# Optimization experiments

Hardware: AMD Instinct MI355X
Metric: run time of the kernel (lower is better)

The kernel has to match this reference:

```python
import jax, jax.numpy as jnp
import numpy as np

N, C, H, W = 8, 32, 48, 48
S, K, OC = 2, 3, 32  # scale_int, kernel_size, out_channels
HID = 256
FEAT = C * K * K  # 288


def setup_inputs() -> dict:
    key = jax.random.key(0)
    ks = jax.random.split(key, 5)
    F_LR = jax.random.normal(ks[0], (N, C, H, W), dtype=jnp.float32)
    v = jax.random.normal(ks[1], (H * S * W * S, 3), dtype=jnp.float32)
    w1 = jax.random.normal(ks[2], (3, HID), dtype=jnp.float32) * 0.2
    b1 = jnp.zeros((HID,), dtype=jnp.float32)
    w2 = jax.random.normal(ks[3], (HID, FEAT * OC), dtype=jnp.float32) * 0.02
    b2 = jnp.zeros((FEAT * OC,), dtype=jnp.float32)
    return {"F_LR": F_LR, "v": v, "w1": w1, "b1": b1, "w2": w2, "b2": b2}


def _unfold(x, k):
    # torch F.unfold(x, k, padding=1): (N, C*k*k, H*W), channel-major then (ki,kj)
    n, c, h, w = x.shape
    xp = jnp.pad(x, ((0, 0), (0, 0), (1, 1), (1, 1)))
    cols = [xp[:, :, i:i + h, j:j + w] for i in range(k) for j in range(k)]
    p = jnp.stack(cols, axis=2)  # (N, C, k*k, H, W)
    return p.reshape(n, c * k * k, h * w)


def reference(F_LR, v, w1, b1, w2, b2):
    n = F_LR.shape[0]
    # weight prediction MLP
    hmid = jax.nn.relu(v @ w1 + b1)
    W_pred = hmid @ w2 + b2  # (H*S*W*S, C*K*K*OC)
    # reshape like torch: view(H,S,W,S,FEAT,OC).permute(1,3,0,2,4,5) -> (S*S, H*W, FEAT, OC)
    Wt = (W_pred.reshape(H, S, W, S, FEAT, OC)
          .transpose(1, 3, 0, 2, 4, 5)
          .reshape(S * S, H * W, FEAT, OC))
    # add_dimensions replicates F_LR S*S times, so patches are shared across p
    pat = _unfold(F_LR, K)  # (N, FEAT, H*W)
    # per-pixel tiny matmul: out[n,p,l,o] = sum_f pat[n,f,l] * Wt[p,l,f,o]
    out = jnp.einsum('nfl,plfo->nplo', pat, Wt)  # (N, S*S, H*W, OC)
    # assemble upsampled image: p=(sh,sw), pixel (h*S+sh, w*S+sw)
    out = (out.reshape(n, S, S, H, W, OC)
           .transpose(0, 5, 3, 1, 4, 2)
           .reshape(n, OC, S * H, S * W))
    # integer scale => create_mask is all-True, masked_select is identity
    return out
```

## Files before the change

kernel.cpp:

```cpp
#include <hip/hip_runtime.h>
#include <hip/hip_bf16.h>

#define NN    8
#define CC    32
#define HH    48
#define WW    48
#define OCC   32
#define HID   256
#define FEAT  288
#define RTOT  9216
#define COLS  9216
#define XUP   96
#define YUP   96
#define OUTSZ (NN*OCC*XUP*YUP)

using bf16x8 = __attribute__((ext_vector_type(8))) __bf16;
using bf16x4 = __attribute__((ext_vector_type(4))) __bf16;
using f32x4  = __attribute__((ext_vector_type(4))) float;

#define GLOAD_LDS16(gp, lp)                                                        \
  __builtin_amdgcn_global_load_lds((const __attribute__((address_space(1))) void*)(gp), \
                                   (__attribute__((address_space(3))) void*)(lp), 16, 0, 0)

__global__ void prep_hmid(const float* __restrict__ v, const float* __restrict__ w1,
                          const float* __restrict__ b1, __hip_bfloat16* __restrict__ hmidp) {
  int r = blockIdx.x;
  int t = threadIdx.x;
  float v0 = v[r*3+0], v1 = v[r*3+1], v2 = v[r*3+2];
  float val = v0*w1[t] + v1*w1[HID+t] + v2*w1[2*HID+t] + b1[t];
  val = fmaxf(val, 0.0f);
  int dst = ((r>>4)*8 + (t>>5))*512 + ((t>>3)&3)*128 + (r&15)*8 + (t&7);
  hmidp[dst] = __float2bfloat16(val);
}

__global__ void prep_w2(const float* __restrict__ w2, __hip_bfloat16* __restrict__ w2p) {
  int idx = blockIdx.x*256 + threadIdx.x;
  int k   = idx / COLS;
  int col = idx % COLS;
  float val = w2[idx];
  int colchunk = col >> 7;
  int cg   = (col >> 4) & 7;
  int lane = (((k>>3)&3)<<4) | (col & 15);
  int kb   = k >> 5;
  int i    = k & 7;
  int dst  = (((colchunk*8 + kb)*8 + cg)*64 + lane)*8 + i;
  w2p[dst] = __float2bfloat16(val);
}

__launch_bounds__(256, 2)
__global__ void fused_main(const float* __restrict__ F_LR,
                           const __hip_bfloat16* __restrict__ hmidp,
                           const __hip_bfloat16* __restrict__ w2p,
                           const float* __restrict__ b2,
                           float* __restrict__ outp,
                           int G, int nch) {
  __shared__ __align__(16) __bf16 pat[CC][3][18][NN];
  __shared__ __align__(16) float  wc[4*OCC*32];
  __shared__ __align__(16) __bf16 Bring[4*4096];
  __shared__ __align__(16) float  biasb[256];
  __shared__ __align__(16) char   dummy[2048];

  const int tid  = threadIdx.x;
  const int lane = tid & 63;
  const int wv   = tid >> 6;
  const int blk  = blockIdx.x;
  const int rowtile = blk / G;
  const int g       = blk - rowtile*G;
  const int X  = rowtile / 3;
  const int Yh = rowtile - X*3;
  const int h  = X >> 1;
  const int w0 = Yh * 16;
  const int l15 = lane & 15;
  const int qt  = lane >> 4;
  const int oc  = lane & 31;
  const int nh  = lane >> 5;
  const int colchunk0 = g*nch;
  const int NT = nch*8;

  const char* w2base = (const char*)w2p + (size_t)colchunk0*65536;
  char* BringB = (char*)Bring;
  auto stage_any = [&](int t) {
    if (t < NT) {
      const char* src = w2base + (size_t)t*8192 + wv*2048 + lane*16;
      char* dst = BringB + (t&3)*8192 + wv*2048;
      GLOAD_LDS16(src, dst);
      GLOAD_LDS16(src + 1024, dst + 1024);
    } else {
      const char* src = w2base + wv*2048 + lane*16;
      GLOAD_LDS16(src, (char*)dummy);
      GLOAD_LDS16(src + 1024, (char*)dummy + 1024);
    }
  };
  stage_any(0); stage_any(1); stage_any(2);
  asm volatile("" ::: "memory");

  bf16x8 a[2][8];
  {
    const bf16x8* ap = reinterpret_cast<const bf16x8*>(hmidp) + (size_t)rowtile*1024 + lane;
    #pragma unroll
    for (int mg = 0; mg < 2; ++mg)
      #pragma unroll
      for (int kb = 0; kb < 8; ++kb) a[mg][kb] = ap[(mg*8 + kb)*64];
  }

  {
    const int n = tid >> 5, c = tid & 31;
    const float* fsrc = F_LR + ((size_t)(n*CC + c)*HH)*WW;
    #pragma unroll
    for (int ki = 0; ki < 3; ++ki) {
      int hh = h - 1 + ki;
      bool hok = (unsigned)hh < (unsigned)HH;
      #pragma unroll
      for (int wi = 0; wi < 18; ++wi) {
        int ww = w0 - 1 + wi;
        float val = (hok && (unsigned)ww < (unsigned)WW) ? fsrc[hh*WW + ww] : 0.f;
        pat[c][ki][wi][n] = (__bf16)val;
      }
    }
  }
  asm volatile("s_waitcnt lgkmcnt(0)" ::: "memory");
  __builtin_amdgcn_sched_barrier(0);
  __builtin_amdgcn_s_barrier();

  float oacc[8][4];
  #pragma unroll
  for (int i = 0; i < 8; ++i)
    { oacc[i][0]=0.f; oacc[i][1]=0.f; oacc[i][2]=0.f; oacc[i][3]=0.f; }

  for (int ch = 0; ch < nch; ++ch) {
    if ((ch & 1) == 0) {
      const char* bsrc = (const char*)(b2 + (size_t)(colchunk0 + ch)*128) + lane*16;
      GLOAD_LDS16(bsrc, (char*)biasb);
    }

    f32x4 acc00 = {0,0,0,0}, acc01 = {0,0,0,0}, acc10 = {0,0,0,0}, acc11 = {0,0,0,0};

    #pragma unroll
    for (int s = 0; s < 8; ++s) {
      const int t = ch*8 + s;
      asm volatile("s_waitcnt vmcnt(4)" ::: "memory");
      const char* bufp = BringB + (size_t)(t&3)*8192 + wv*2048;
      bf16x8 b0 = *(const bf16x8*)(bufp + lane*16);
      bf16x8 b1 = *(const bf16x8*)(bufp + 1024 + lane*16);
      stage_any(t + 3);
      acc00 = __builtin_amdgcn_mfma_f32_16x16x32_bf16(a[0][s], b0, acc00, 0,0,0);
      acc01 = __builtin_amdgcn_mfma_f32_16x16x32_bf16(a[0][s], b1, acc01, 0,0,0);
      acc10 = __builtin_amdgcn_mfma_f32_16x16x32_bf16(a[1][s], b0, acc10, 0,0,0);
      acc11 = __builtin_amdgcn_mfma_f32_16x16x32_bf16(a[1][s], b1, acc11, 0,0,0);
    }

    asm volatile("s_waitcnt vmcnt(6)" ::: "memory");
    {
      float bias0 = biasb[(ch&1)*128 + wv*32 + l15];
      float bias1 = biasb[(ch&1)*128 + wv*32 + 16 + l15];
      #pragma unroll
      for (int mg = 0; mg < 2; ++mg) {
        #pragma unroll
        for (int ng = 0; ng < 2; ++ng) {
          f32x4 A = (mg==0) ? (ng==0?acc00:acc01) : (ng==0?acc10:acc11);
          float bb = ng ? bias1 : bias0;
          A[0]+=bb; A[1]+=bb; A[2]+=bb; A[3]+=bb;
          int ocx  = ng*16 + l15;
          int ridx = (mg*16 + qt*4) ^ ((ocx&7)<<2);
          *(f32x4*)&wc[wv*1024 + ocx*32 + ridx] = A;
        }
      }
    }
    asm volatile("s_waitcnt lgkmcnt(0)" ::: "memory");
    __builtin_amdgcn_sched_barrier(0);
    __builtin_amdgcn_s_barrier();

    const int swz = (oc & 7) << 2;
    #pragma unroll
    for (int fl = 0; fl < 4; ++fl) {
      const int f   = (colchunk0 + ch)*4 + fl;
      const int c   = f / 9;
      const int rem = f - c*9;
      const int ki  = rem / 3;
      const int kj  = rem - ki*3;
      const f32x4 wlo = *(const f32x4*)&wc[fl*1024 + oc*32 + ((wv*8    ) ^ swz)];
      const f32x4 whi = *(const f32x4*)&wc[fl*1024 + oc*32 + ((wv*8 + 4) ^ swz)];
      const __bf16* pbase = &pat[c][ki][0][0] + nh*4;
      #pragma unroll
      for (int rrh = 0; rrh < 4; ++rrh) {
        bf16x4 pq = *(const bf16x4*)(pbase + (wv*4 + rrh + kj)*8);
        float w0v = (rrh < 2) ? ((rrh == 0) ? wlo[0] : wlo[2]) : ((rrh == 2) ? whi[0] : whi[2]);
        float w1v = (rrh < 2) ? ((rrh == 0) ? wlo[1] : wlo[3]) : ((rrh == 2) ? whi[1] : whi[3]);
        #pragma unroll
        for (int q = 0; q < 4; ++q) {
          float pv = (float)pq[q];
          oacc[rrh*2][q]   += w0v * pv;
          oacc[rrh*2+1][q] += w1v * pv;
        }
      }
    }
    asm volatile("s_waitcnt lgkmcnt(0)" ::: "memory");
    __builtin_amdgcn_sched_barrier(0);
    __builtin_amdgcn_s_barrier();
  }

  float* OP = outp + (size_t)g*OUTSZ;
  #pragma unroll
  for (int q = 0; q < 4; ++q) {
    int n = nh*4 + q;
    f32x4 v0, v1;
    v0[0]=oacc[0][q]; v0[1]=oacc[1][q]; v0[2]=oacc[2][q]; v0[3]=oacc[3][q];
    v1[0]=oacc[4][q]; v1[1]=oacc[5][q]; v1[2]=oacc[6][q]; v1[3]=oacc[7][q];
    float* dst = OP + (((size_t)(n*OCC + oc)*XUP + X)*YUP + Yh*32 + wv*8);
    *(f32x4*)dst     = v0;
    *(f32x4*)(dst+4) = v1;
  }
}

__global__ void reduce2(const float* __restrict__ P, float* __restrict__ out) {
  int i = blockIdx.x*256 + threadIdx.x;
  if (i < OUTSZ/4) {
    f32x4 a = ((const f32x4*)P)[i];
    f32x4 b = ((const f32x4*)(P + OUTSZ))[i];
    ((f32x4*)out)[i] = a + b;
  }
}

extern "C" void kernel_launch(void* const* d_in, const int* in_sizes, int n_in,
                              void* d_out, int out_size, void* d_ws, size_t ws_size,
                              hipStream_t stream) {
  const float* F_LR = (const float*)d_in[0];
  const float* v    = (const float*)d_in[1];
  const float* w1   = (const float*)d_in[2];
  const float* b1   = (const float*)d_in[3];
  const float* w2   = (const float*)d_in[4];
  const float* b2   = (const float*)d_in[5];
  float* out = (float*)d_out;

  const size_t prepBytes = (size_t)RTOT*HID*2;
  const size_t need2 = 2*prepBytes + 2ull*OUTSZ*4;
  const int G   = (ws_size >= need2) ? 2 : 1;
  const int nch = 72 / G;

  __hip_bfloat16* hmidp = (__hip_bfloat16*)d_ws;
  __hip_bfloat16* w2p   = (__hip_bfloat16*)((char*)d_ws + prepBytes);
  float* P = (float*)((char*)d_ws + 2*prepBytes);
  float* target = (G == 2) ? P : out;

  hipLaunchKernelGGL(prep_hmid, dim3(RTOT), dim3(HID), 0, stream, v, w1, b1, hmidp);
  hipLaunchKernelGGL(prep_w2,   dim3((HID*COLS)/256), dim3(256), 0, stream, w2, w2p);
  hipLaunchKernelGGL(fused_main, dim3(288*G), dim3(256), 0, stream,
                     F_LR, hmidp, w2p, b2, target, G, nch);
  if (G == 2)
    hipLaunchKernelGGL(reduce2, dim3(OUTSZ/4/256), dim3(256), 0, stream, P, out);
}
```

Before: 199.9 us.

## Software-pipeline LDS B loads, raise MFMA priority, pack FMAs, coalesce patch staging

Restructures the MFMA inner loop so each step's B fragments are read from LDS one step ahead into double-buffered registers. The next global-to-LDS stage is issued after the MFMAs, and the MFMA group runs under raised wave priority. The per-pixel FMA accumulation uses 2-wide float vectors so the compiler can emit packed FMA, and patch loading becomes a flat strided loop for more coalesced global reads. The aim is to hide LDS latency behind MFMA work and cut ALU instruction count. In exchange it uses more registers and relies on delicate waitcnt counts, which could be off and cause stalls or races.

```diff
diff --git a/kernel.cpp b/kernel.cpp
--- a/kernel.cpp
+++ b/kernel.cpp
@@ -17,6 +17,7 @@
 using bf16x8 = __attribute__((ext_vector_type(8))) __bf16;
 using bf16x4 = __attribute__((ext_vector_type(4))) __bf16;
 using f32x4  = __attribute__((ext_vector_type(4))) float;
+using f32x2  = __attribute__((ext_vector_type(2))) float;
 
 #define GLOAD_LDS16(gp, lp)                                                        \
   __builtin_amdgcn_global_load_lds((const __attribute__((address_space(1))) void*)(gp), \
@@ -103,31 +104,34 @@
       for (int kb = 0; kb < 8; ++kb) a[mg][kb] = ap[(mg*8 + kb)*64];
   }
 
-  {
-    const int n = tid >> 5, c = tid & 31;
-    const float* fsrc = F_LR + ((size_t)(n*CC + c)*HH)*WW;
-    #pragma unroll
-    for (int ki = 0; ki < 3; ++ki) {
-      int hh = h - 1 + ki;
-      bool hok = (unsigned)hh < (unsigned)HH;
-      #pragma unroll
-      for (int wi = 0; wi < 18; ++wi) {
-        int ww = w0 - 1 + wi;
-        float val = (hok && (unsigned)ww < (unsigned)WW) ? fsrc[hh*WW + ww] : 0.f;
-        pat[c][ki][wi][n] = (__bf16)val;
-      }
-    }
+  for (int idx = tid; idx < NN*CC*3*18; idx += 256) {
+    int wi = idx % 18;
+    int t2 = idx / 18;
+    int ki = t2 % 3;
+    int t3 = t2 / 3;
+    int c  = t3 & 31;
+    int n  = t3 >> 5;
+    int hh = h - 1 + ki;
+    int ww = w0 - 1 + wi;
+    float val = 0.f;
+    if ((unsigned)hh < (unsigned)HH && (unsigned)ww < (unsigned)WW)
+      val = F_LR[((n*CC + c)*HH + hh)*WW + ww];
+    pat[c][ki][wi][n] = (__bf16)val;
   }
   asm volatile("s_waitcnt lgkmcnt(0)" ::: "memory");
   __builtin_amdgcn_sched_barrier(0);
   __builtin_amdgcn_s_barrier();
 
-  float oacc[8][4];
+  f32x2 oacc2[8][2];
   #pragma unroll
-  for (int i = 0; i < 8; ++i)
-    { oacc[i][0]=0.f; oacc[i][1]=0.f; oacc[i][2]=0.f; oacc[i][3]=0.f; }
+  for (int i = 0; i < 8; ++i) { oacc2[i][0] = 0.f; oacc2[i][1] = 0.f; }
+
+  auto ldb = [&](int u, int off) -> bf16x8 {
+    return *(const bf16x8*)(BringB + (size_t)(u&3)*8192 + wv*2048 + off + lane*16);
+  };
 
   for (int ch = 0; ch < nch; ++ch) {
+    const int t0 = ch*8;
     if ((ch & 1) == 0) {
       const char* bsrc = (const char*)(b2 + (size_t)(colchunk0 + ch)*128) + lane*16;
       GLOAD_LDS16(bsrc, (char*)biasb);
@@ -135,18 +139,31 @@
 
     f32x4 acc00 = {0,0,0,0}, acc01 = {0,0,0,0}, acc10 = {0,0,0,0}, acc11 = {0,0,0,0};
 
+    asm volatile("s_waitcnt vmcnt(4)" ::: "memory");
+    bf16x8 b0A = ldb(t0, 0),   b1A = ldb(t0, 1024);
+    stage_any(t0 + 3);
+    asm volatile("s_waitcnt vmcnt(4)" ::: "memory");
+    bf16x8 b0B = ldb(t0+1, 0), b1B = ldb(t0+1, 1024);
+    asm volatile("s_waitcnt lgkmcnt(2)" ::: "memory");
+    stage_any(t0 + 4);
+
     #pragma unroll
     for (int s = 0; s < 8; ++s) {
-      const int t = ch*8 + s;
-      asm volatile("s_waitcnt vmcnt(4)" ::: "memory");
-      const char* bufp = BringB + (size_t)(t&3)*8192 + wv*2048;
-      bf16x8 b0 = *(const bf16x8*)(bufp + lane*16);
-      bf16x8 b1 = *(const bf16x8*)(bufp + 1024 + lane*16);
-      stage_any(t + 3);
-      acc00 = __builtin_amdgcn_mfma_f32_16x16x32_bf16(a[0][s], b0, acc00, 0,0,0);
-      acc01 = __builtin_amdgcn_mfma_f32_16x16x32_bf16(a[0][s], b1, acc01, 0,0,0);
-      acc10 = __builtin_amdgcn_mfma_f32_16x16x32_bf16(a[1][s], b0, acc10, 0,0,0);
-      acc11 = __builtin_amdgcn_mfma_f32_16x16x32_bf16(a[1][s], b1, acc11, 0,0,0);
+      const bf16x8 cb0 = (s & 1) ? b0B : b0A;
+      const bf16x8 cb1 = (s & 1) ? b1B : b1A;
+      __builtin_amdgcn_s_setprio(1);
+      acc00 = __builtin_amdgcn_mfma_f32_16x16x32_bf16(a[0][s], cb0, acc00, 0,0,0);
+      acc01 = __builtin_amdgcn_mfma_f32_16x16x32_bf16(a[0][s], cb1, acc01, 0,0,0);
+      acc10 = __builtin_amdgcn_mfma_f32_16x16x32_bf16(a[1][s], cb0, acc10, 0,0,0);
+      acc11 = __builtin_amdgcn_mfma_f32_16x16x32_bf16(a[1][s], cb1, acc11, 0,0,0);
+      __builtin_amdgcn_s_setprio(0);
+      if (s < 6) {
+        asm volatile("s_waitcnt vmcnt(4)" ::: "memory");
+        if (s & 1) { b0B = ldb(t0+s+2, 0); b1B = ldb(t0+s+2, 1024); }
+        else       { b0A = ldb(t0+s+2, 0); b1A = ldb(t0+s+2, 1024); }
+        asm volatile("s_waitcnt lgkmcnt(2)" ::: "memory");
+        stage_any(t0 + s + 5);
+      }
     }
 
     asm volatile("s_waitcnt vmcnt(6)" ::: "memory");
@@ -184,14 +201,14 @@
       #pragma unroll
       for (int rrh = 0; rrh < 4; ++rrh) {
         bf16x4 pq = *(const bf16x4*)(pbase + (wv*4 + rrh + kj)*8);
+        f32x2 p01; p01[0] = (float)pq[0]; p01[1] = (float)pq[1];
+        f32x2 p23; p23[0] = (float)pq[2]; p23[1] = (float)pq[3];
         float w0v = (rrh < 2) ? ((rrh == 0) ? wlo[0] : wlo[2]) : ((rrh == 2) ? whi[0] : whi[2]);
         float w1v = (rrh < 2) ? ((rrh == 0) ? wlo[1] : wlo[3]) : ((rrh == 2) ? whi[1] : whi[3]);
-        #pragma unroll
-        for (int q = 0; q < 4; ++q) {
-          float pv = (float)pq[q];
-          oacc[rrh*2][q]   += w0v * pv;
-          oacc[rrh*2+1][q] += w1v * pv;
-        }
+        oacc2[rrh*2][0]   += p01 * w0v;
+        oacc2[rrh*2][1]   += p23 * w0v;
+        oacc2[rrh*2+1][0] += p01 * w1v;
+        oacc2[rrh*2+1][1] += p23 * w1v;
       }
     }
     asm volatile("s_waitcnt lgkmcnt(0)" ::: "memory");
@@ -204,8 +221,10 @@
   for (int q = 0; q < 4; ++q) {
     int n = nh*4 + q;
     f32x4 v0, v1;
-    v0[0]=oacc[0][q]; v0[1]=oacc[1][q]; v0[2]=oacc[2][q]; v0[3]=oacc[3][q];
-    v1[0]=oacc[4][q]; v1[1]=oacc[5][q]; v1[2]=oacc[6][q]; v1[3]=oacc[7][q];
+    v0[0]=oacc2[0][q>>1][q&1]; v0[1]=oacc2[1][q>>1][q&1];
+    v0[2]=oacc2[2][q>>1][q&1]; v0[3]=oacc2[3][q>>1][q&1];
+    v1[0]=oacc2[4][q>>1][q&1]; v1[1]=oacc2[5][q>>1][q&1];
+    v1[2]=oacc2[6][q>>1][q&1]; v1[3]=oacc2[7][q>>1][q&1];
     float* dst = OP + (((size_t)(n*OCC + oc)*XUP + X)*YUP + Yh*32 + wv*8);
     *(f32x4*)dst     = v0;
     *(f32x4*)(dst+4) = v1;
```

Measured after the change: 213.6 us. +6.8%, slower.
